# Kernel optimization log

Measured on AMD Instinct MI355X. Metric: run time of the kernel, lower is better.

Reference implementation:

```python
import jax, jax.numpy as jnp
import numpy as np

N, F, H, ES, EG, G, NC = 32768, 64, 4, 524288, 524288, 64, 10
BN_EPS = 1e-5


def setup_inputs():
    key = jax.random.key(0)
    ks = jax.random.split(key, 24)
    return {
        "x": jax.random.normal(ks[0], (N, F), jnp.float32),
        "edge_index": jax.random.randint(ks[1], (2, EG), 0, N),
        "batch": jnp.sort(jax.random.randint(ks[2], (N,), 0, G)),
        "scatter_idx": jax.random.randint(ks[3], (4, 2, ES), 0, N),
        "scatter_attr": jax.random.normal(ks[4], (4, ES), jnp.float32),
        "gat_W": jax.random.normal(ks[5], (4, F, H * F), jnp.float32) * 0.1,
        "gat_asrc": jax.random.normal(ks[6], (4, H, F), jnp.float32) * 0.1,
        "gat_adst": jax.random.normal(ks[7], (4, H, F), jnp.float32) * 0.1,
        "gat_b": jax.random.normal(ks[8], (4, H * F), jnp.float32) * 0.01,
        "mlp_W": jax.random.normal(ks[9], (4, H * F, F), jnp.float32) * 0.06,
        "mlp_b": jnp.zeros((4, F), jnp.float32),
        "mlp_g": jnp.ones((4, F), jnp.float32),
        "mlp_beta": jnp.zeros((4, F), jnp.float32),
        "fc1_W": jax.random.normal(ks[10], (F, 256), jnp.float32) * 0.1,
        "fc1_b": jnp.zeros((256,), jnp.float32),
        "fc1_g": jnp.ones((256,), jnp.float32),
        "fc1_beta": jnp.zeros((256,), jnp.float32),
        "fc2_W": jax.random.normal(ks[11], (256, 128), jnp.float32) * 0.06,
        "fc2_b": jnp.zeros((128,), jnp.float32),
        "fc2_g": jnp.ones((128,), jnp.float32),
        "fc2_beta": jnp.zeros((128,), jnp.float32),
        "fc3_W": jax.random.normal(ks[12], (128, NC), jnp.float32) * 0.08,
        "fc3_b": jnp.zeros((NC,), jnp.float32),
        "fc3_g": jnp.ones((NC,), jnp.float32),
        "fc3_beta": jnp.zeros((NC,), jnp.float32),
    }


def _solo_pass(idx, attr, x):
    # message: edge_attr * x[src]; aggregate: scatter-add at dst
    src, dst = idx[0], idx[1]
    return jax.ops.segment_sum(attr[:, None] * x[src], dst, num_segments=x.shape[0])


def _batchnorm(y, g, b):
    # training-mode BatchNorm1d: batch stats, biased variance
    mu = jnp.mean(y, axis=0)
    var = jnp.mean((y - mu) ** 2, axis=0)
    return (y - mu) * jax.lax.rsqrt(var + BN_EPS) * g + b


def _gat(x, W, asrc, adst, bias, src, dst):
    n = x.shape[0]
    h = (x @ W).reshape(n, H, F)                     # [N,H,F]
    a_s = jnp.sum(h * asrc, axis=-1)                 # [N,H]
    a_d = jnp.sum(h * adst, axis=-1)                 # [N,H]
    loop = jnp.arange(n)
    s2 = jnp.concatenate([src, loop])                # add self-loops (PyG default)
    d2 = jnp.concatenate([dst, loop])
    e = jax.nn.leaky_relu(a_s[s2] + a_d[d2], 0.2)    # [E2,H]
    m = jax.ops.segment_max(e, d2, num_segments=n)
    ex = jnp.exp(e - m[d2])
    denom = jax.ops.segment_sum(ex, d2, num_segments=n)
    alpha = ex / denom[d2]                           # softmax over in-edges of each dst
    out = jax.ops.segment_sum(alpha[:, :, None] * h[s2], d2, num_segments=n)
    return out.reshape(n, H * F) + bias              # concat heads + bias


def reference(x, edge_index, batch, scatter_idx, scatter_attr,
              gat_W, gat_asrc, gat_adst, gat_b, mlp_W, mlp_b, mlp_g, mlp_beta,
              fc1_W, fc1_b, fc1_g, fc1_beta, fc2_W, fc2_b, fc2_g, fc2_beta,
              fc3_W, fc3_b, fc3_g, fc3_beta):
    src, dst = edge_index[0], edge_index[1]
    x0 = _solo_pass(scatter_idx[0], scatter_attr[0], x)
    xh1 = jnp.abs(_solo_pass(scatter_idx[1], scatter_attr[1], x))
    xh2 = jnp.abs(_solo_pass(scatter_idx[2], scatter_attr[2], x))
    xh3 = jnp.abs(_solo_pass(scatter_idx[3], scatter_attr[3], x))
    x1 = _solo_pass(scatter_idx[0], scatter_attr[0], xh1)
    x2 = _solo_pass(scatter_idx[0], scatter_attr[0], xh2)
    x3 = _solo_pass(scatter_idx[0], scatter_attr[0], xh3)
    xs = [x0, x1, x2, x3]
    for i in range(4):
        g = _gat(xs[i], gat_W[i], gat_asrc[i], gat_adst[i], gat_b[i], src, dst)
        z = jax.nn.elu(g) @ mlp_W[i] + mlp_b[i]      # (dropout = identity in eval)
        xs[i] = _batchnorm(z, mlp_g[i], mlp_beta[i])
    x_stage1 = x + xs[0]
    x_stage2 = x_stage1 + xs[1] + xs[2] + xs[3]
    pooled = jax.ops.segment_sum(x_stage2, batch, num_segments=G)  # global_add_pool
    h1 = jax.nn.relu(_batchnorm(pooled @ fc1_W + fc1_b, fc1_g, fc1_beta))
    h2 = jax.nn.relu(_batchnorm(h1 @ fc2_W + fc2_b, fc2_g, fc2_beta))
    out = _batchnorm(h2 @ fc3_W + fc3_b, fc3_g, fc3_beta)
    return out
```

## Files before the change

kernel.cpp:

```cpp
#include <hip/hip_runtime.h>
#include <hip/hip_bf16.h>

#define N_NODES 32768
#define F_DIM 64
#define H_HEADS 4
#define HF 256
#define ES_EDGES 524288
#define EG_EDGES 524288
#define G_GRAPHS 64
#define NC_OUT 10
#define BN_EPS 1e-5f
#define NH (N_NODES * H_HEADS)
#define NF_ELEMS (N_NODES * F_DIM)
#define CAP 48
#define NBIN 64
#define BSTRIDE 8960

typedef short bf16x8 __attribute__((ext_vector_type(8)));
typedef float f32x4 __attribute__((ext_vector_type(4)));

__device__ __forceinline__ float eluf(float x) { return x > 0.f ? x : expm1f(x); }
__device__ __forceinline__ float lreluf(float x) { return x > 0.f ? x : 0.2f * x; }
__device__ __forceinline__ float bu2f(unsigned short v) {
    return __uint_as_float((unsigned)v << 16);
}
__device__ __forceinline__ unsigned short f2bu(float f) {
    union { __hip_bfloat16 b; unsigned short u; } cv;
    cv.b = __float2bfloat16(f);
    return cv.u;
}

struct P5i { const int* p[5]; };
struct P5f { const float* p[5]; };

__global__ __launch_bounds__(256) void k_binA_prep(
        P5i src, P5i dst, P5f attr, int* __restrict__ gcur,
        long long* __restrict__ staging,
        const float* __restrict__ gat_W, const float* __restrict__ mlp_W,
        unsigned short* __restrict__ gat_Wt, unsigned short* __restrict__ mlp_Wt,
        const float* __restrict__ x, unsigned short* __restrict__ xbf,
        const float* __restrict__ gat_asrc, const float* __restrict__ gat_adst,
        float* __restrict__ ws, float* __restrict__ wd) {
    int b = blockIdx.x;
    if (b < 2560) {
        __shared__ int hist[NBIN];
        __shared__ int base[NBIN];
        int g = b >> 9;
        int e0 = (b & 511) * 1024 + threadIdx.x;
        const int* dp = dst.p[g];
        const int* sp = src.p[g];
        const float* ap = attr.p[g];
        int d[4], s[4], bin[4];
        unsigned av[4];
#pragma unroll
        for (int k = 0; k < 4; ++k) {
            int e = e0 + k * 256;
            d[k] = dp[e]; s[k] = sp[e];
            av[k] = ap ? __float_as_uint(ap[e]) : 0u;
            bin[k] = d[k] >> 9;
        }
        if (threadIdx.x < NBIN) hist[threadIdx.x] = 0;
        __syncthreads();
#pragma unroll
        for (int k = 0; k < 4; ++k) atomicAdd(&hist[bin[k]], 1);
        __syncthreads();
        if (threadIdx.x < NBIN) {
            base[threadIdx.x] = atomicAdd(&gcur[g * NBIN + threadIdx.x],
                                          hist[threadIdx.x]);
            hist[threadIdx.x] = 0;
        }
        __syncthreads();
#pragma unroll
        for (int k = 0; k < 4; ++k) {
            int p = atomicAdd(&hist[bin[k]], 1);
            int pos = base[bin[k]] + p;
            if (pos < BSTRIDE) {
                long long rec = ((long long)av[k] << 32) |
                                (unsigned)(s[k] | ((d[k] & 0x1FF) << 15));
                staging[((size_t)g * NBIN + bin[k]) * BSTRIDE + pos] = rec;
            }
        }
    } else if (b < 3072) {
        int t = ((b - 2560) << 8) + threadIdx.x;
        if (t < 65536) {
            int layer = t >> 14, r = t & 16383;
            int n = r >> 6, k = r & 63;
            gat_Wt[t] = f2bu(gat_W[(size_t)layer * 16384 + k * 256 + n]);
        } else {
            int u = t - 65536;
            int layer = u >> 14, r = u & 16383;
            int n = r >> 8, k = r & 255;
            mlp_Wt[(size_t)layer * 16384 + r] =
                f2bu(mlp_W[(size_t)layer * 16384 + k * 64 + n]);
        }
    } else if (b < 5120) {
        int t = ((b - 3072) << 8) + threadIdx.x;
        float4 v = ((const float4*)x)[t];
        ushort4 o;
        o.x = f2bu(v.x); o.y = f2bu(v.y); o.z = f2bu(v.z); o.w = f2bu(v.w);
        ((ushort4*)xbf)[t] = o;
    } else {
        int q = b - 5120;
        int l = q >> 1, sel = q & 1;
        int h = threadIdx.x >> 6, k = threadIdx.x & 63;
        const float* Wl = gat_W + (size_t)l * 16384;
        const float* av = (sel ? gat_adst : gat_asrc) + l * 256 + h * 64;
        float s = 0.f;
#pragma unroll 8
        for (int f = 0; f < 64; ++f) s += Wl[k * 256 + h * 64 + f] * av[f];
        (sel ? wd : ws)[(l * 4 + h) * 64 + k] = s;
    }
}

__global__ __launch_bounds__(1024) void k_binB(
        const long long* __restrict__ staging, const int* __restrict__ gcur,
        int* __restrict__ cnt, int* __restrict__ bg0,
        long long* __restrict__ brecs) {
    __shared__ int lcnt[512];
    int g = blockIdx.x / NBIN;
    int bin = blockIdx.x % NBIN;
    if (threadIdx.x < 512) lcnt[threadIdx.x] = 0;
    __syncthreads();
    int cb = gcur[g * NBIN + bin];
    cb = cb < BSTRIDE ? cb : BSTRIDE;
    const long long* st = staging + ((size_t)g * NBIN + bin) * BSTRIDE;
    for (int idx = threadIdx.x; idx < cb; idx += 1024) {
        long long rec = st[idx];
        unsigned lo = (unsigned)rec;
        int s = lo & 0x7FFF;
        int dlow = (lo >> 15) & 0x1FF;
        int p = atomicAdd(&lcnt[dlow], 1);
        if (p >= CAP) continue;
        int d = (bin << 9) | dlow;
        if (g == 0) {
            bg0[d * CAP + p] = s;
        } else {
            long long r = (rec & 0xFFFFFFFF00000000ll) | (unsigned)s;
            brecs[((size_t)(g - 1) * N_NODES + d) * CAP + p] = r;
        }
    }
    __syncthreads();
    if (threadIdx.x < 512)
        cnt[g * N_NODES + (bin << 9) + threadIdx.x] = lcnt[threadIdx.x];
}

__global__ void k_sgather3(const ushort4* __restrict__ xb4, const int* __restrict__ cnt,
                           const int2* __restrict__ brecs, ushort4* __restrict__ xh4) {
    int g = blockIdx.y;
    int d = blockIdx.x * 4 + (threadIdx.x >> 6);
    int lane = threadIdx.x & 63;
    int chunk = lane & 15, quad = lane >> 4;
    int c = cnt[(g + 2) * N_NODES + d];
    c = c < CAP ? c : CAP;
    const int2* rec = brecs + ((size_t)(g + 1) * N_NODES + d) * CAP;
    float a0 = 0.f, a1 = 0.f, a2 = 0.f, a3 = 0.f;
    for (int j0 = 0; j0 < c; j0 += 4) {
        int j = j0 + quad;
        if (j < c) {
            int2 r = rec[j];
            float w = __int_as_float(r.y);
            ushort4 hv = xb4[(size_t)r.x * 16 + chunk];
            a0 += w * bu2f(hv.x); a1 += w * bu2f(hv.y);
            a2 += w * bu2f(hv.z); a3 += w * bu2f(hv.w);
        }
    }
    a0 += __shfl_xor(a0, 16); a0 += __shfl_xor(a0, 32);
    a1 += __shfl_xor(a1, 16); a1 += __shfl_xor(a1, 32);
    a2 += __shfl_xor(a2, 16); a2 += __shfl_xor(a2, 32);
    a3 += __shfl_xor(a3, 16); a3 += __shfl_xor(a3, 32);
    if (quad == 0) {
        ushort4 o;
        o.x = f2bu(a0); o.y = f2bu(a1); o.z = f2bu(a2); o.w = f2bu(a3);
        xh4[(size_t)g * (NF_ELEMS / 4) + d * 16 + chunk] = o;
    }
}

__global__ void k_sgather_quad(const ushort4* __restrict__ xb4,
                               const ushort4* __restrict__ xh4,
                               const int* __restrict__ cnt, const int2* __restrict__ brecs,
                               ushort4* __restrict__ xs4,
                               const float* __restrict__ wsg, const float* __restrict__ wdg,
                               float* __restrict__ a_s_all, float* __restrict__ a_d_all) {
    __shared__ float WS[1024], WD[1024];
    for (int i = threadIdx.x; i < 1024; i += 256) { WS[i] = wsg[i]; WD[i] = wdg[i]; }
    __syncthreads();
    int d = blockIdx.x * 4 + (threadIdx.x >> 6);
    int lane = threadIdx.x & 63;
    int chunk = lane & 15, quad = lane >> 4;
    int c = cnt[1 * N_NODES + d];
    c = c < CAP ? c : CAP;
    const int2* rec = brecs + (size_t)d * CAP;
    const ushort4* base = (quad == 0) ? xb4 : (xh4 + (size_t)(quad - 1) * (NF_ELEMS / 4));
    float a0 = 0.f, a1 = 0.f, a2 = 0.f, a3 = 0.f;
    int j = 0;
    for (; j + 2 <= c; j += 2) {
        int2 r0 = rec[j], r1 = rec[j + 1];
        float w0 = __int_as_float(r0.y), w1 = __int_as_float(r1.y);
        ushort4 h0 = base[(size_t)r0.x * 16 + chunk];
        ushort4 h1 = base[(size_t)r1.x * 16 + chunk];
        float v00 = bu2f(h0.x), v01 = bu2f(h0.y), v02 = bu2f(h0.z), v03 = bu2f(h0.w);
        float v10 = bu2f(h1.x), v11 = bu2f(h1.y), v12 = bu2f(h1.z), v13 = bu2f(h1.w);
        if (quad) {
            v00 = fabsf(v00); v01 = fabsf(v01); v02 = fabsf(v02); v03 = fabsf(v03);
            v10 = fabsf(v10); v11 = fabsf(v11); v12 = fabsf(v12); v13 = fabsf(v13);
        }
        a0 += w0 * v00 + w1 * v10; a1 += w0 * v01 + w1 * v11;
        a2 += w0 * v02 + w1 * v12; a3 += w0 * v03 + w1 * v13;
    }
    for (; j < c; ++j) {
        int2 r = rec[j];
        float w = __int_as_float(r.y);
        ushort4 h0 = base[(size_t)r.x * 16 + chunk];
        float v0 = bu2f(h0.x), v1 = bu2f(h0.y), v2 = bu2f(h0.z), v3 = bu2f(h0.w);
        if (quad) { v0 = fabsf(v0); v1 = fabsf(v1); v2 = fabsf(v2); v3 = fabsf(v3); }
        a0 += w * v0; a1 += w * v1; a2 += w * v2; a3 += w * v3;
    }
    const float* wsq = WS + quad * 256;
    const float* wdq = WD + quad * 256;
    float lsv[4], ldv[4];
#pragma unroll
    for (int h = 0; h < 4; ++h) {
        int o = h * 64 + chunk * 4;
        lsv[h] = a0 * wsq[o] + a1 * wsq[o + 1] + a2 * wsq[o + 2] + a3 * wsq[o + 3];
        ldv[h] = a0 * wdq[o] + a1 * wdq[o + 1] + a2 * wdq[o + 2] + a3 * wdq[o + 3];
    }
#pragma unroll
    for (int h = 0; h < 4; ++h) {
        lsv[h] += __shfl_xor(lsv[h], 1); lsv[h] += __shfl_xor(lsv[h], 2);
        lsv[h] += __shfl_xor(lsv[h], 4); lsv[h] += __shfl_xor(lsv[h], 8);
        ldv[h] += __shfl_xor(ldv[h], 1); ldv[h] += __shfl_xor(ldv[h], 2);
        ldv[h] += __shfl_xor(ldv[h], 4); ldv[h] += __shfl_xor(ldv[h], 8);
    }
    if (chunk == 0) {
        float4 vs; vs.x = lsv[0]; vs.y = lsv[1]; vs.z = lsv[2]; vs.w = lsv[3];
        ((float4*)a_s_all)[(size_t)quad * N_NODES + d] = vs;
        float4 vd; vd.x = ldv[0]; vd.y = ldv[1]; vd.z = ldv[2]; vd.w = ldv[3];
        ((float4*)a_d_all)[(size_t)quad * N_NODES + d] = vd;
    }
    ushort4 o;
    o.x = f2bu(a0); o.y = f2bu(a1); o.z = f2bu(a2); o.w = f2bu(a3);
    xs4[(size_t)quad * (NF_ELEMS / 4) + d * 16 + chunk] = o;
}

__global__ __launch_bounds__(256) void k_gat_mlp(
        const int* __restrict__ cnt, const int* __restrict__ bg0,
        const float* __restrict__ a_s_all, const float* __restrict__ a_d_all,
        const ushort4* __restrict__ xs4_all, const unsigned short* __restrict__ gWt,
        const float* __restrict__ gat_b,
        const unsigned short* __restrict__ mWt_all, const float* __restrict__ mlp_b,
        float* __restrict__ z4, float* __restrict__ sums_all,
        float* __restrict__ sumsq_all) {
    __shared__ float ESa[16 * 49 * 4];
    __shared__ unsigned short EScol[16 * 50];
    __shared__ unsigned short AG[16 * 268];
    unsigned short* A2s = (unsigned short*)ESa;

    int lb = ((blockIdx.x & 7) << 10) | (blockIdx.x >> 3);
    int L = lb >> 11;
    int bx = lb & 2047;
    const float* a_sc = a_s_all + (size_t)L * N_NODES * 4;
    const float* a_dc = a_d_all + (size_t)L * N_NODES * 4;
    const ushort4* xs4 = xs4_all + (size_t)L * (NF_ELEMS / 4);
    const unsigned short* xsu = (const unsigned short*)xs4;
    const unsigned short* gWtL = gWt + (size_t)L * 16384;
    const float* gat_bL = gat_b + L * HF;
    const unsigned short* mWt = mWt_all + (size_t)L * 16384;
    const float* mbias = mlp_b + L * F_DIM;
    float* z = z4 + (size_t)L * NF_ELEMS;
    float* sums = sums_all + L * 64;
    float* sumsq = sumsq_all + L * 64;

    int wid = threadIdx.x >> 6, lane = threadIdx.x & 63;
    int dbase = bx * 16;
    int quad = lane >> 4;
    int e16 = lane & 15;
    for (int k = 0; k < 4; ++k) {
        int drow = wid * 4 + k;
        int d = dbase + drow;
        int c = cnt[d];
        c = c < CAP ? c : CAP;
        const int* col = bg0 + (size_t)d * CAP;
        float a_dd = a_dc[d * 4 + quad];
        float e_self = lreluf(a_sc[d * 4 + quad] + a_dd);
        float m = e_self;
        float ext[3]; int st[3];
#pragma unroll
        for (int t = 0; t < 3; ++t) {
            int j = t * 16 + e16;
            if (j < c) {
                int s = col[j];
                st[t] = s;
                float e = lreluf(a_sc[s * 4 + quad] + a_dd);
                ext[t] = e;
                m = fmaxf(m, e);
            } else { st[t] = 0; ext[t] = 0.f; }
        }
        m = fmaxf(m, __shfl_xor(m, 1)); m = fmaxf(m, __shfl_xor(m, 2));
        m = fmaxf(m, __shfl_xor(m, 4)); m = fmaxf(m, __shfl_xor(m, 8));
        float dsum = 0.f;
#pragma unroll
        for (int t = 0; t < 3; ++t) {
            float ex = (t * 16 + e16 < c) ? __expf(ext[t] - m) : 0.f;
            ext[t] = ex;
            dsum += ex;
        }
        dsum += __shfl_xor(dsum, 1); dsum += __shfl_xor(dsum, 2);
        dsum += __shfl_xor(dsum, 4); dsum += __shfl_xor(dsum, 8);
        float exs = __expf(e_self - m);
        float inv = 1.f / (dsum + exs);
        float* ESrow = ESa + drow * 49 * 4;
        unsigned short* ECrow = EScol + drow * 50;
#pragma unroll
        for (int t = 0; t < 3; ++t) {
            int j = t * 16 + e16;
            if (j < c) {
                ESrow[j * 4 + quad] = ext[t] * inv;
                if (quad == 0) ECrow[j] = (unsigned short)st[t];
            }
        }
        if (e16 == 0) ESrow[c * 4 + quad] = exs * inv;
        if (lane == 0) ECrow[c] = (unsigned short)d;
        int f = lane;
        float ag0 = 0.f, ag1 = 0.f, ag2 = 0.f, ag3 = 0.f;
        int cl = c + 1;
        int j = 0;
        for (; j + 2 <= cl; j += 2) {
            f32x4 al0 = *(const f32x4*)(ESrow + j * 4);
            f32x4 al1 = *(const f32x4*)(ESrow + j * 4 + 4);
            unsigned s0 = ECrow[j];
            unsigned s1 = ECrow[j + 1];
            float x0 = bu2f(xsu[s0 * 64u + (unsigned)f]);
            float x1 = bu2f(xsu[s1 * 64u + (unsigned)f]);
            ag0 += al0[0] * x0 + al1[0] * x1;
            ag1 += al0[1] * x0 + al1[1] * x1;
            ag2 += al0[2] * x0 + al1[2] * x1;
            ag3 += al0[3] * x0 + al1[3] * x1;
        }
        if (j < cl) {
            f32x4 al0 = *(const f32x4*)(ESrow + j * 4);
            unsigned s0 = ECrow[j];
            float x0 = bu2f(xsu[s0 * 64u + (unsigned)f]);
            ag0 += al0[0] * x0; ag1 += al0[1] * x0;
            ag2 += al0[2] * x0; ag3 += al0[3] * x0;
        }
        unsigned short* AGrow = AG + drow * 268;
        AGrow[f]       = f2bu(ag0);
        AGrow[64 + f]  = f2bu(ag1);
        AGrow[128 + f] = f2bu(ag2);
        AGrow[192 + f] = f2bu(ag3);
    }
    __syncthreads();
    {
        const unsigned short* agp = AG + e16 * 268 + wid * 64 + quad * 8;
        bf16x8 af0 = *(const bf16x8*)agp;
        bf16x8 af1 = *(const bf16x8*)(agp + 32);
#pragma unroll
        for (int nt = 0; nt < 4; ++nt) {
            int ng = wid * 64 + nt * 16 + e16;
            const unsigned short* bp = gWtL + (size_t)ng * 64 + quad * 8;
            bf16x8 b0 = *(const bf16x8*)bp;
            bf16x8 b1 = *(const bf16x8*)(bp + 32);
            f32x4 cc = {0.f, 0.f, 0.f, 0.f};
            cc = __builtin_amdgcn_mfma_f32_16x16x32_bf16(af0, b0, cc, 0, 0, 0);
            cc = __builtin_amdgcn_mfma_f32_16x16x32_bf16(af1, b1, cc, 0, 0, 0);
            float gb = gat_bL[ng];
#pragma unroll
            for (int r = 0; r < 4; ++r) {
                float v = eluf(cc[r] + gb);
                A2s[(quad * 4 + r) * 268 + ng] = f2bu(v);
            }
        }
    }
    __syncthreads();
    int n = lane & 15;
    f32x4 acc = {0.f, 0.f, 0.f, 0.f};
    const unsigned short* ap = A2s + n * 268 + quad * 8;
    const unsigned short* wtp = mWt + (size_t)(wid * 16 + n) * 256 + quad * 8;
#pragma unroll
    for (int ka = 0; ka < 8; ++ka) {
        bf16x8 af = *(const bf16x8*)(ap + ka * 32);
        bf16x8 bfr = *(const bf16x8*)(wtp + ka * 32);
        acc = __builtin_amdgcn_mfma_f32_16x16x32_bf16(af, bfr, acc, 0, 0, 0);
    }
    float b = mbias[wid * 16 + n];
    float s = 0.f, sq = 0.f;
#pragma unroll
    for (int r = 0; r < 4; ++r) {
        float v = acc[r] + b;
        z[(size_t)(dbase + quad * 4 + r) * 64 + wid * 16 + n] = v;
        s += v; sq += v * v;
    }
    s += __shfl_xor(s, 16); s += __shfl_xor(s, 32);
    sq += __shfl_xor(sq, 16); sq += __shfl_xor(sq, 32);
    if (quad == 0) {
        unsafeAtomicAdd(&sums[wid * 16 + n], s);
        unsafeAtomicAdd(&sumsq[wid * 16 + n], sq);
    }
}

__global__ void k_bnpool(const float* __restrict__ x, const float* __restrict__ z4,
                         const float* __restrict__ sums, const float* __restrict__ sumsq,
                         const float* __restrict__ g, const float* __restrict__ beta,
                         const int* __restrict__ batch, float* __restrict__ pooled) {
    int col = threadIdx.x & 63, rg = threadIdx.x >> 6;
    const float invN = 1.f / (float)N_NODES;
    float sc[4], off[4];
#pragma unroll
    for (int i = 0; i < 4; ++i) {
        float mu = sums[i * 64 + col] * invN;
        float var = sumsq[i * 64 + col] * invN - mu * mu;
        sc[i] = g[i * 64 + col] * rsqrtf(var + BN_EPS);
        off[i] = beta[i * 64 + col] - mu * sc[i];
    }
    float offt = off[0] + off[1] + off[2] + off[3];
    int r0 = blockIdx.x * 128 + rg * 32;
    int cur = -1;
    float acc = 0.f;
    for (int r = r0; r < r0 + 32; ++r) {
        int gb = batch[r];
        if (gb != cur) {
            if (cur >= 0) unsafeAtomicAdd(&pooled[cur * 64 + col], acc);
            cur = gb; acc = 0.f;
        }
        float v = x[(size_t)r * 64 + col] + offt;
#pragma unroll
        for (int i = 0; i < 4; ++i)
            v += sc[i] * z4[(size_t)i * NF_ELEMS + (size_t)r * 64 + col];
        acc += v;
    }
    if (cur >= 0) unsafeAtomicAdd(&pooled[cur * 64 + col], acc);
}

__global__ void k_h1(const float* __restrict__ pooled, const float* __restrict__ W1,
                     const float* __restrict__ b1, float* __restrict__ h1p) {
    int o = blockIdx.x * 256 + threadIdx.x;
    int m = o >> 8, n = o & 255;
    float s = b1[n];
#pragma unroll 8
    for (int k = 0; k < 64; ++k) s += pooled[m * 64 + k] * W1[k * 256 + n];
    h1p[o] = s;
}

__global__ __launch_bounds__(256) void k_h2(
        const float* __restrict__ h1p, const float* __restrict__ g1,
        const float* __restrict__ be1, const float* __restrict__ W2,
        const float* __restrict__ b2, float* __restrict__ h2p) {
    __shared__ float sT[256 * 65];
    __shared__ float sc[256], off[256];
    int t = threadIdx.x;
    for (int o = t; o < 16384; o += 256) {
        int m = o >> 8, k = o & 255;
        sT[k * 65 + m] = h1p[o];
    }
    __syncthreads();
    {
        int colc = t;
        float s = 0.f, sq = 0.f;
        for (int m = 0; m < 64; ++m) { float v = sT[colc * 65 + m]; s += v; sq += v * v; }
        float mu = s * (1.f / 64.f);
        float var = sq * (1.f / 64.f) - mu * mu;
        float scl = g1[colc] * rsqrtf(var + BN_EPS);
        sc[colc] = scl; off[colc] = be1[colc] - mu * scl;
    }
    __syncthreads();
    int m = t & 63, nl = t >> 6;
    int n = blockIdx.x * 4 + nl;
    float s = b2[n];
    for (int k = 0; k < 256; ++k) {
        float h = fmaxf(sT[k * 65 + m] * sc[k] + off[k], 0.f);
        s += h * W2[k * 128 + n];
    }
    h2p[m * 128 + n] = s;
}

__global__ __launch_bounds__(1024) void k_h3(
        const float* __restrict__ h2p, const float* __restrict__ g2,
        const float* __restrict__ be2, const float* __restrict__ W3,
        const float* __restrict__ b3, const float* __restrict__ g3,
        const float* __restrict__ be3, float* __restrict__ out) {
    __shared__ float sT[128 * 65];
    __shared__ float sc[128], off[128];
    __shared__ float h3[64 * NC_OUT];
    __shared__ float sc3[NC_OUT], off3[NC_OUT];
    int t = threadIdx.x;
    for (int o = t; o < 8192; o += 1024) {
        int m = o >> 7, k = o & 127;
        sT[k * 65 + m] = h2p[o];
    }
    __syncthreads();
    if (t < 128) {
        float s = 0.f, sq = 0.f;
        for (int m = 0; m < 64; ++m) { float v = sT[t * 65 + m]; s += v; sq += v * v; }
        float mu = s * (1.f / 64.f);
        float var = sq * (1.f / 64.f) - mu * mu;
        float scl = g2[t] * rsqrtf(var + BN_EPS);
        sc[t] = scl; off[t] = be2[t] - mu * scl;
    }
    __syncthreads();
    for (int o = t; o < 8192; o += 1024) {
        int m = o & 63, k = o >> 6;
        sT[k * 65 + m] = fmaxf(sT[k * 65 + m] * sc[k] + off[k], 0.f);
    }
    __syncthreads();
    if (t < 64 * NC_OUT) {
        int m = t / NC_OUT, n = t % NC_OUT;
        float s = b3[n];
        for (int k = 0; k < 128; ++k) s += sT[k * 65 + m] * W3[k * NC_OUT + n];
        h3[t] = s;
    }
    __syncthreads();
    if (t < NC_OUT) {
        float s = 0.f, sq = 0.f;
        for (int m = 0; m < 64; ++m) { float v = h3[m * NC_OUT + t]; s += v; sq += v * v; }
        float mu = s * (1.f / 64.f);
        float var = sq * (1.f / 64.f) - mu * mu;
        float scl = g3[t] * rsqrtf(var + BN_EPS);
        sc3[t] = scl; off3[t] = be3[t] - mu * scl;
    }
    __syncthreads();
    if (t < 64 * NC_OUT) out[t] = h3[t] * sc3[t % NC_OUT] + off3[t % NC_OUT];
}

extern "C" void kernel_launch(void* const* d_in, const int* in_sizes, int n_in,
                              void* d_out, int out_size, void* d_ws, size_t ws_size,
                              hipStream_t stream) {
    const float* x        = (const float*)d_in[0];
    const int*   ei       = (const int*)d_in[1];
    const int*   batch    = (const int*)d_in[2];
    const int*   sidx     = (const int*)d_in[3];
    const float* sattr    = (const float*)d_in[4];
    const float* gat_W    = (const float*)d_in[5];
    const float* gat_asrc = (const float*)d_in[6];
    const float* gat_adst = (const float*)d_in[7];
    const float* gat_b    = (const float*)d_in[8];
    const float* mlp_W    = (const float*)d_in[9];
    const float* mlp_b    = (const float*)d_in[10];
    const float* mlp_g    = (const float*)d_in[11];
    const float* mlp_beta = (const float*)d_in[12];
    const float* fc1_W    = (const float*)d_in[13];
    const float* fc1_b    = (const float*)d_in[14];
    const float* fc1_g    = (const float*)d_in[15];
    const float* fc1_beta = (const float*)d_in[16];
    const float* fc2_W    = (const float*)d_in[17];
    const float* fc2_b    = (const float*)d_in[18];
    const float* fc2_g    = (const float*)d_in[19];
    const float* fc2_beta = (const float*)d_in[20];
    const float* fc3_W    = (const float*)d_in[21];
    const float* fc3_b    = (const float*)d_in[22];
    const float* fc3_g    = (const float*)d_in[23];
    const float* fc3_beta = (const float*)d_in[24];

    char* wp = (char*)d_ws;
    auto alloc = [&](size_t bytes) {
        char* r = wp;
        wp += (bytes + 255) & ~(size_t)255;
        return (void*)r;
    };
    unsigned short* xs_bf = (unsigned short*)alloc(4 * (size_t)NF_ELEMS * 2);
    float* a_s_all = (float*)alloc(4 * (size_t)N_NODES * 4 * 4);
    float* a_d_all = (float*)alloc(4 * (size_t)N_NODES * 4 * 4);
    float* ws = (float*)alloc(1024 * 4);
    float* wd = (float*)alloc(1024 * 4);
    int*   cnt    = (int*)alloc(5 * N_NODES * 4);
    int*   gcur   = (int*)alloc(5 * NBIN * 4);
    float* sums   = (float*)alloc(4 * 64 * 4);
    float* sumsq  = (float*)alloc(4 * 64 * 4);
    float* pooled = (float*)alloc(G_GRAPHS * F_DIM * 4);
    const size_t ZBYTES = (5 * N_NODES + 5 * NBIN + 2 * 4 * 64 + G_GRAPHS * F_DIM) * 4;
    int*   bg0    = (int*)alloc((size_t)N_NODES * CAP * 4);
    unsigned short* gat_Wt = (unsigned short*)alloc(4 * 64 * 256 * 2);
    unsigned short* mlp_Wt = (unsigned short*)alloc(4 * 256 * 64 * 2);
    float* h1p = (float*)alloc(64 * 256 * 4);
    float* h2p = (float*)alloc(64 * 128 * 4);
    long long* staging = (long long*)alloc(5 * (size_t)NBIN * BSTRIDE * 8);
    char* U1 = (char*)alloc(4 * (size_t)NF_ELEMS * 2);
    unsigned short* xbf = (unsigned short*)U1;
    unsigned short* xh  = (unsigned short*)(U1 + (size_t)NF_ELEMS * 2);
    char* U2 = (char*)alloc(4 * (size_t)N_NODES * CAP * 8);
    long long* brecs = (long long*)U2;
    float* z4 = (float*)U2;

    P5i srcs, dsts; P5f attrs;
    srcs.p[0] = ei;              dsts.p[0] = ei + EG_EDGES;          attrs.p[0] = nullptr;
    for (int i = 0; i < 4; ++i) {
        srcs.p[i + 1]  = sidx + (size_t)i * 2 * ES_EDGES;
        dsts.p[i + 1]  = sidx + (size_t)i * 2 * ES_EDGES + ES_EDGES;
        attrs.p[i + 1] = sattr + (size_t)i * ES_EDGES;
    }

    hipMemsetAsync(cnt, 0, ZBYTES, stream);
    k_binA_prep<<<5128, 256, 0, stream>>>(srcs, dsts, attrs, gcur, staging,
                                          gat_W, mlp_W, gat_Wt, mlp_Wt, x, xbf,
                                          gat_asrc, gat_adst, ws, wd);

    k_binB<<<5 * NBIN, 1024, 0, stream>>>(staging, gcur, cnt, bg0, brecs);

    k_sgather3<<<dim3(N_NODES / 4, 3), 256, 0, stream>>>(
        (const ushort4*)xbf, cnt, (const int2*)brecs, (ushort4*)xh);
    k_sgather_quad<<<N_NODES / 4, 256, 0, stream>>>(
        (const ushort4*)xbf, (const ushort4*)xh, cnt, (const int2*)brecs,
        (ushort4*)xs_bf, ws, wd, a_s_all, a_d_all);

    k_gat_mlp<<<8192, 256, 0, stream>>>(
        cnt, bg0, a_s_all, a_d_all, (const ushort4*)xs_bf, gat_Wt, gat_b,
        mlp_Wt, mlp_b, z4, sums, sumsq);

    k_bnpool<<<256, 256, 0, stream>>>(x, z4, sums, sumsq, mlp_g, mlp_beta,
                                      batch, pooled);
    k_h1<<<64, 256, 0, stream>>>(pooled, fc1_W, fc1_b, h1p);
    k_h2<<<32, 256, 0, stream>>>(h1p, fc1_g, fc1_beta, fc2_W, fc2_b, h2p);
    k_h3<<<1, 1024, 0, stream>>>(h2p, fc2_g, fc2_beta, fc3_W, fc3_b,
                                 fc3_g, fc3_beta, (float*)d_out);
}
```

Measured before the change: 487.6 us.

## Interleave four destination rows per wave in GAT attention and aggregation

Restructures the GAT attention and aggregation loop so each wave processes its four destination rows together instead of one after another. Neighbor index loads, logits, max/sum reductions and the gather loop are batched across the rows to expose more independent memory loads and hide gather latency. Attention weights are now stored as bf16 in a smaller shared buffer, padded up to the longest of the four rows, which shrinks LDS use. In exchange it uses more registers, does wasted gather work on rows shorter than the longest, and lowers the precision of the attention coefficients.

```diff
diff --git a/kernel.cpp b/kernel.cpp
--- a/kernel.cpp
+++ b/kernel.cpp
@@ -250,10 +250,11 @@
         const unsigned short* __restrict__ mWt_all, const float* __restrict__ mlp_b,
         float* __restrict__ z4, float* __restrict__ sums_all,
         float* __restrict__ sumsq_all) {
-    __shared__ float ESa[16 * 49 * 4];
-    __shared__ unsigned short EScol[16 * 50];
-    __shared__ unsigned short AG[16 * 268];
-    unsigned short* A2s = (unsigned short*)ESa;
+    __shared__ __align__(16) unsigned short BUF[16 * 268];
+    __shared__ __align__(16) unsigned short AG[16 * 268];
+    unsigned short* ESa = BUF;
+    unsigned short* ECol = BUF + 3200;
+    unsigned short* A2s = BUF;
 
     int lb = ((blockIdx.x & 7) << 10) | (blockIdx.x >> 3);
     int L = lb >> 11;
@@ -274,80 +275,110 @@
     int dbase = bx * 16;
     int quad = lane >> 4;
     int e16 = lane & 15;
+    int f = lane;
+
+    int dA[4], cA[4]; float addA[4];
+#pragma unroll
     for (int k = 0; k < 4; ++k) {
-        int drow = wid * 4 + k;
-        int d = dbase + drow;
-        int c = cnt[d];
-        c = c < CAP ? c : CAP;
-        const int* col = bg0 + (size_t)d * CAP;
-        float a_dd = a_dc[d * 4 + quad];
-        float e_self = lreluf(a_sc[d * 4 + quad] + a_dd);
-        float m = e_self;
-        float ext[3]; int st[3];
+        dA[k] = dbase + wid * 4 + k;
+        int c = cnt[dA[k]];
+        cA[k] = c < CAP ? c : CAP;
+        addA[k] = a_dc[dA[k] * 4 + quad];
+    }
+    int stA[4][3];
+#pragma unroll
+    for (int k = 0; k < 4; ++k)
 #pragma unroll
         for (int t = 0; t < 3; ++t) {
             int j = t * 16 + e16;
-            if (j < c) {
-                int s = col[j];
-                st[t] = s;
-                float e = lreluf(a_sc[s * 4 + quad] + a_dd);
-                ext[t] = e;
-                m = fmaxf(m, e);
-            } else { st[t] = 0; ext[t] = 0.f; }
-        }
-        m = fmaxf(m, __shfl_xor(m, 1)); m = fmaxf(m, __shfl_xor(m, 2));
-        m = fmaxf(m, __shfl_xor(m, 4)); m = fmaxf(m, __shfl_xor(m, 8));
-        float dsum = 0.f;
+            stA[k][t] = (j < cA[k]) ? bg0[(size_t)dA[k] * CAP + j] : dA[k];
+        }
+    float exA[4][3], eslf[4], mA[4];
+#pragma unroll
+    for (int k = 0; k < 4; ++k) {
+        eslf[k] = lreluf(a_sc[dA[k] * 4 + quad] + addA[k]);
+        mA[k] = eslf[k];
 #pragma unroll
         for (int t = 0; t < 3; ++t) {
-            float ex = (t * 16 + e16 < c) ? __expf(ext[t] - m) : 0.f;
-            ext[t] = ex;
-            dsum += ex;
-        }
-        dsum += __shfl_xor(dsum, 1); dsum += __shfl_xor(dsum, 2);
-        dsum += __shfl_xor(dsum, 4); dsum += __shfl_xor(dsum, 8);
-        float exs = __expf(e_self - m);
-        float inv = 1.f / (dsum + exs);
-        float* ESrow = ESa + drow * 49 * 4;
-        unsigned short* ECrow = EScol + drow * 50;
+            float e = lreluf(a_sc[stA[k][t] * 4 + quad] + addA[k]);
+            e = (t * 16 + e16 < cA[k]) ? e : -1e30f;
+            exA[k][t] = e;
+            mA[k] = fmaxf(mA[k], e);
+        }
+    }
+#pragma unroll
+    for (int k = 0; k < 4; ++k) {
+        mA[k] = fmaxf(mA[k], __shfl_xor(mA[k], 1));
+        mA[k] = fmaxf(mA[k], __shfl_xor(mA[k], 2));
+        mA[k] = fmaxf(mA[k], __shfl_xor(mA[k], 4));
+        mA[k] = fmaxf(mA[k], __shfl_xor(mA[k], 8));
+    }
+    float dsA[4];
+#pragma unroll
+    for (int k = 0; k < 4; ++k) {
+        float ds = 0.f;
+#pragma unroll
+        for (int t = 0; t < 3; ++t) {
+            exA[k][t] = __expf(exA[k][t] - mA[k]);
+            ds += exA[k][t];
+        }
+        dsA[k] = ds;
+    }
+#pragma unroll
+    for (int k = 0; k < 4; ++k) {
+        dsA[k] += __shfl_xor(dsA[k], 1); dsA[k] += __shfl_xor(dsA[k], 2);
+        dsA[k] += __shfl_xor(dsA[k], 4); dsA[k] += __shfl_xor(dsA[k], 8);
+    }
+#pragma unroll
+    for (int k = 0; k < 4; ++k) {
+        float exs = __expf(eslf[k] - mA[k]);
+        float inv = 1.f / (dsA[k] + exs);
+        int drow = wid * 4 + k;
+        unsigned short* ESrow = ESa + drow * 200;
+        unsigned short* ECrow = ECol + drow * 50;
 #pragma unroll
         for (int t = 0; t < 3; ++t) {
             int j = t * 16 + e16;
-            if (j < c) {
-                ESrow[j * 4 + quad] = ext[t] * inv;
-                if (quad == 0) ECrow[j] = (unsigned short)st[t];
-            }
-        }
-        if (e16 == 0) ESrow[c * 4 + quad] = exs * inv;
-        if (lane == 0) ECrow[c] = (unsigned short)d;
-        int f = lane;
-        float ag0 = 0.f, ag1 = 0.f, ag2 = 0.f, ag3 = 0.f;
-        int cl = c + 1;
-        int j = 0;
-        for (; j + 2 <= cl; j += 2) {
-            f32x4 al0 = *(const f32x4*)(ESrow + j * 4);
-            f32x4 al1 = *(const f32x4*)(ESrow + j * 4 + 4);
-            unsigned s0 = ECrow[j];
-            unsigned s1 = ECrow[j + 1];
-            float x0 = bu2f(xsu[s0 * 64u + (unsigned)f]);
-            float x1 = bu2f(xsu[s1 * 64u + (unsigned)f]);
-            ag0 += al0[0] * x0 + al1[0] * x1;
-            ag1 += al0[1] * x0 + al1[1] * x1;
-            ag2 += al0[2] * x0 + al1[2] * x1;
-            ag3 += al0[3] * x0 + al1[3] * x1;
-        }
-        if (j < cl) {
-            f32x4 al0 = *(const f32x4*)(ESrow + j * 4);
-            unsigned s0 = ECrow[j];
-            float x0 = bu2f(xsu[s0 * 64u + (unsigned)f]);
-            ag0 += al0[0] * x0; ag1 += al0[1] * x0;
-            ag2 += al0[2] * x0; ag3 += al0[3] * x0;
-        }
-        unsigned short* AGrow = AG + drow * 268;
-        AGrow[f]       = f2bu(ag0);
-        AGrow[64 + f]  = f2bu(ag1);
-        AGrow[128 + f] = f2bu(ag2);
-        AGrow[192 + f] = f2bu(ag3);
+            ESrow[j * 4 + quad] = f2bu(exA[k][t] * inv);
+            if (quad == 0) ECrow[j] = (unsigned short)stA[k][t];
+        }
+        if (e16 == 1) {
+            ESrow[48 * 4 + quad] = 0;
+            if (quad == 0) ECrow[48] = (unsigned short)dA[k];
+        }
+        if (e16 == 0) {
+            ESrow[cA[k] * 4 + quad] = f2bu(exs * inv);
+            if (quad == 0) ECrow[cA[k]] = (unsigned short)dA[k];
+        }
+    }
+    int mx01 = cA[0] > cA[1] ? cA[0] : cA[1];
+    int mx23 = cA[2] > cA[3] ? cA[2] : cA[3];
+    int mx = (mx01 > mx23 ? mx01 : mx23) + 1;
+    float ag[4][4];
+#pragma unroll
+    for (int k = 0; k < 4; ++k)
+#pragma unroll
+        for (int h = 0; h < 4; ++h) ag[k][h] = 0.f;
+    for (int j = 0; j < mx; ++j) {
+#pragma unroll
+        for (int k = 0; k < 4; ++k) {
+            int drow = wid * 4 + k;
+            uint2 p = ((const uint2*)(ESa + drow * 200))[j];
+            unsigned s = ECol[drow * 50 + j];
+            float x0 = bu2f(xsu[(size_t)s * 64 + f]);
+            ag[k][0] += __uint_as_float(p.x << 16) * x0;
+            ag[k][1] += __uint_as_float(p.x & 0xFFFF0000u) * x0;
+            ag[k][2] += __uint_as_float(p.y << 16) * x0;
+            ag[k][3] += __uint_as_float(p.y & 0xFFFF0000u) * x0;
+        }
+    }
+#pragma unroll
+    for (int k = 0; k < 4; ++k) {
+        unsigned short* AGrow = AG + (wid * 4 + k) * 268;
+        AGrow[f]       = f2bu(ag[k][0]);
+        AGrow[64 + f]  = f2bu(ag[k][1]);
+        AGrow[128 + f] = f2bu(ag[k][2]);
+        AGrow[192 + f] = f2bu(ag[k][3]);
     }
     __syncthreads();
     {
```

After: 453.5 us. -7.0%, faster.
